# Performance work log

Measured on AMD Instinct MI355X. Metric: run time of the kernel, lower is better.

Reference implementation:

```python
import jax, jax.numpy as jnp
import numpy as np

B, C, T_TEXT, T_FEAT = 16, 192, 512, 2048
DUR_MAX = 8


def setup_inputs() -> dict:
    key = jax.random.key(0)
    k1, k2 = jax.random.split(key)
    x = jax.random.normal(k1, (B, C, T_TEXT), dtype=jnp.float32)
    w = jax.random.randint(k2, (B, T_TEXT), 0, DUR_MAX, dtype=jnp.int32)
    x_mask = jnp.ones((B, T_TEXT), dtype=jnp.float32)
    y_mask = jnp.ones((B, T_FEAT), dtype=jnp.float32)
    return {"x": x, "w": w, "x_mask": x_mask, "y_mask": y_mask}


def _alignment_path(w, x_mask, t_feat):
    # w: (B, T_text) int durations. Builds one-hot path (B, T_feat, T_text):
    # path[b, j, i] = 1 iff cum_w[i-1] <= j < cum_w[i]
    wm = (w.astype(jnp.float32) * x_mask).astype(jnp.int32)  # mask durations
    cum = jnp.cumsum(wm, axis=-1)                            # (B, T_text)
    frames = jnp.arange(t_feat, dtype=jnp.int32)             # (T_feat,)
    lt = (frames[None, :, None] < cum[:, None, :]).astype(jnp.float32)  # (B, T_feat, T_text)
    # subtract shifted-by-one along text axis -> one-hot per frame
    path = lt - jnp.pad(lt[:, :, :-1], ((0, 0), (0, 0), (1, 0)))
    return path


def reference(x, w, x_mask, y_mask):
    # x: (B, C, T_text) -> (B, C, T_feat)
    t_feat = y_mask.shape[-1]
    path = _alignment_path(w, x_mask, t_feat)                # (B, T_feat, T_text)
    xm = x * x_mask[:, None, :]
    y = jnp.einsum("bci,bji->bcj", xm, path)                 # duplicate by duration
    return y * y_mask[:, None, :]
```

## Files before the change

### kernel.cpp

```cpp
#include <hip/hip_runtime.h>


#define BB 16
#define CC 192
#define T_TEXT 512
#define T_FEAT 2048
#define CH_TILE 12
#define NTILES (CC / CH_TILE)
#define NTHREADS 1024

__global__ __launch_bounds__(NTHREADS) void dup_by_dur_fused(
    const float* __restrict__ x, const int* __restrict__ w,
    const float* __restrict__ x_mask, const float* __restrict__ y_mask,
    float* __restrict__ out)
{
    const int t    = threadIdx.x;
    const int lane = t & 63;
    const int wv   = t >> 6;
    const int b    = blockIdx.x >> 4;
    const int tile = blockIdx.x & 15;

    __shared__ int   wtot[16];
    __shared__ short sidx[T_FEAT];
    __shared__ float sxm[T_FEAT];

    *(int*)(sidx + 2 * t) = 0;
    *(float2*)(sxm + 2 * t) = float2{0.f, 0.f};

    int wm = 0; float xm = 0.f;
    if (t < T_TEXT) {
        float wf = (float)w[b * T_TEXT + t];
        xm = x_mask[b * T_TEXT + t];
        wm = (int)(wf * xm);
    }

    int p = wm;
    #pragma unroll
    for (int off = 1; off < 64; off <<= 1) {
        int v = __shfl_up(p, off);
        if (lane >= off) p += v;
    }
    if (lane == 63) wtot[wv] = p;
    __syncthreads();

    if (t < T_TEXT) {
        int prefix = 0;
        #pragma unroll
        for (int k = 0; k < T_TEXT / 64; ++k)
            if (k < wv) prefix += wtot[k];
        int end   = prefix + p;
        int start = end - wm;
        start = min(start, T_FEAT);
        end   = min(end, T_FEAT);
        for (int j = start; j < end; ++j) { sidx[j] = (short)t; sxm[j] = xm; }
    }
    __syncthreads();

    const int j  = 4 * (t & 511);
    const int ch = t >> 9;
    const short4 i4 = *(const short4*)(sidx + j);
    float4 s4 = *(const float4*)(sxm + j);
    const float4 ym = *(const float4*)(y_mask + (size_t)b * T_FEAT + j);
    s4.x *= ym.x; s4.y *= ym.y; s4.z *= ym.z; s4.w *= ym.w;

    const int cbase = tile * CH_TILE + ch;
    #pragma unroll
    for (int k = 0; k < CH_TILE / 2; ++k) {
        const int c = cbase + 2 * k;
        const float* __restrict__ xr = x + ((size_t)b * CC + c) * T_TEXT;
        float* __restrict__ orow = out + ((size_t)b * CC + c) * T_FEAT;
        float4 o;
        o.x = xr[i4.x] * s4.x;
        o.y = xr[i4.y] * s4.y;
        o.z = xr[i4.z] * s4.z;
        o.w = xr[i4.w] * s4.w;
        *(float4*)(orow + j) = o;
    }
}

extern "C" void kernel_launch(void* const* d_in, const int* in_sizes, int n_in,
                              void* d_out, int out_size, void* d_ws, size_t ws_size,
                              hipStream_t stream) {
    const float* x      = (const float*)d_in[0];
    const int*   w      = (const int*)d_in[1];
    const float* x_mask = (const float*)d_in[2];
    const float* y_mask = (const float*)d_in[3];
    float* out = (float*)d_out;

    dup_by_dur_fused<<<BB * NTILES, NTHREADS, 0, stream>>>(x, w, x_mask, y_mask, out);
}
```

Measured before the change: 13.16 us.

## Stage masked x channel tile in LDS and gather from shared memory

Each block now loads its 12-channel slice of x into a padded LDS buffer up front and applies x_mask there. The duration-expanded gather then reads from LDS instead of doing scattered global loads. Unfilled frames point to an extra zero column, which replaces the per-frame mask array, and the y_mask load is hoisted to the top so it overlaps the scan. The cost is about 25 KB more LDS per block and float4 LDS accesses at odd row offsets (row stride 513), which may be misaligned or split.

Result: slower. 13.47 us (+2.3%).

```diff
diff --git a/kernel.cpp b/kernel.cpp
--- a/kernel.cpp
+++ b/kernel.cpp
@@ -8,6 +8,7 @@
 #define CH_TILE 12
 #define NTILES (CC / CH_TILE)
 #define NTHREADS 1024
+#define SXROW 513
 
 __global__ __launch_bounds__(NTHREADS) void dup_by_dur_fused(
     const float* __restrict__ x, const int* __restrict__ w,
@@ -19,20 +20,31 @@
     const int wv   = t >> 6;
     const int b    = blockIdx.x >> 4;
     const int tile = blockIdx.x & 15;
+    const int cglob0 = tile * CH_TILE;
 
     __shared__ int   wtot[16];
+    __shared__ float sxm_tok[T_TEXT];
     __shared__ short sidx[T_FEAT];
-    __shared__ float sxm[T_FEAT];
+    __shared__ float sx[CH_TILE * SXROW];
 
-    *(int*)(sidx + 2 * t) = 0;
-    *(float2*)(sxm + 2 * t) = float2{0.f, 0.f};
+    const int cA = t >> 7, iA = (t & 127) * 4;
+    const float4 xa = *(const float4*)(x + ((size_t)b * CC + cglob0 + cA) * T_TEXT + iA);
+    const int qB = t + NTHREADS;
+    const int cB = qB >> 7, iB = (qB & 127) * 4;
+    float4 xb = float4{0.f, 0.f, 0.f, 0.f};
+    if (t < 512)
+        xb = *(const float4*)(x + ((size_t)b * CC + cglob0 + cB) * T_TEXT + iB);
+    const float4 ym = *(const float4*)(y_mask + (size_t)b * T_FEAT + 4 * (t & 511));
 
     int wm = 0; float xm = 0.f;
     if (t < T_TEXT) {
         float wf = (float)w[b * T_TEXT + t];
         xm = x_mask[b * T_TEXT + t];
         wm = (int)(wf * xm);
+        sxm_tok[t] = xm;
     }
+
+    *(int*)(sidx + 2 * t) = 0x02000200;
 
     int p = wm;
     #pragma unroll
@@ -43,6 +55,20 @@
     if (lane == 63) wtot[wv] = p;
     __syncthreads();
 
+    {
+        const float4 mA = *(const float4*)(sxm_tok + iA);
+        float4 v = xa;
+        v.x *= mA.x; v.y *= mA.y; v.z *= mA.z; v.w *= mA.w;
+        *(float4*)(sx + cA * SXROW + iA) = v;
+        if (t < 512) {
+            const float4 mB = *(const float4*)(sxm_tok + iB);
+            float4 u = xb;
+            u.x *= mB.x; u.y *= mB.y; u.z *= mB.z; u.w *= mB.w;
+            *(float4*)(sx + cB * SXROW + iB) = u;
+        }
+        if (t < CH_TILE) sx[t * SXROW + 512] = 0.f;
+    }
+
     if (t < T_TEXT) {
         int prefix = 0;
         #pragma unroll
@@ -52,29 +78,25 @@
         int start = end - wm;
         start = min(start, T_FEAT);
         end   = min(end, T_FEAT);
-        for (int j = start; j < end; ++j) { sidx[j] = (short)t; sxm[j] = xm; }
+        for (int j = start; j < end; ++j) sidx[j] = (short)t;
     }
     __syncthreads();
 
     const int j  = 4 * (t & 511);
     const int ch = t >> 9;
     const short4 i4 = *(const short4*)(sidx + j);
-    float4 s4 = *(const float4*)(sxm + j);
-    const float4 ym = *(const float4*)(y_mask + (size_t)b * T_FEAT + j);
-    s4.x *= ym.x; s4.y *= ym.y; s4.z *= ym.z; s4.w *= ym.w;
+    const int o0 = (int)i4.x, o1 = (int)i4.y, o2 = (int)i4.z, o3 = (int)i4.w;
 
-    const int cbase = tile * CH_TILE + ch;
     #pragma unroll
     for (int k = 0; k < CH_TILE / 2; ++k) {
-        const int c = cbase + 2 * k;
-        const float* __restrict__ xr = x + ((size_t)b * CC + c) * T_TEXT;
-        float* __restrict__ orow = out + ((size_t)b * CC + c) * T_FEAT;
+        const int c = 2 * k + ch;
+        const float* __restrict__ row = sx + c * SXROW;
         float4 o;
-        o.x = xr[i4.x] * s4.x;
-        o.y = xr[i4.y] * s4.y;
-        o.z = xr[i4.z] * s4.z;
-        o.w = xr[i4.w] * s4.w;
-        *(float4*)(orow + j) = o;
+        o.x = row[o0] * ym.x;
+        o.y = row[o1] * ym.y;
+        o.z = row[o2] * ym.z;
+        o.w = row[o3] * ym.w;
+        *(float4*)(out + ((size_t)b * CC + cglob0 + c) * T_FEAT + j) = o;
     }
 }
 
```
